# Optimization experiments

Hardware: AMD Instinct MI355X
Metric: run time of the kernel (lower is better)

## Reference

```python
import jax, jax.numpy as jnp
import numpy as np

N_NODES = 100000
N_EDGES = 3200000
N_FEAT = 512
HIDDEN = 16
OUT_DIM = 1


def setup_inputs() -> dict:
    key = jax.random.key(0)
    ks = jax.random.split(key, 6)
    x = jax.random.normal(ks[0], (N_NODES, N_FEAT), dtype=jnp.float32)
    lap_vals = jax.random.uniform(ks[1], (N_EDGES,), dtype=jnp.float32)
    W1 = jax.random.normal(ks[2], (N_FEAT, HIDDEN), dtype=jnp.float32) * 0.05
    b1 = jnp.zeros((HIDDEN,), dtype=jnp.float32)
    W2 = jax.random.normal(ks[3], (HIDDEN, OUT_DIM), dtype=jnp.float32) * 0.05
    b2 = jnp.zeros((OUT_DIM,), dtype=jnp.float32)
    lap_rows = jax.random.randint(ks[4], (N_EDGES,), 0, N_NODES, dtype=jnp.int32)
    lap_cols = jax.random.randint(ks[5], (N_EDGES,), 0, N_NODES, dtype=jnp.int32)
    return {"x": x, "lap_vals": lap_vals, "W1": W1, "b1": b1,
            "W2": W2, "b2": b2, "lap_rows": lap_rows, "lap_cols": lap_cols}


def _spmm(vals, rows, cols, dense):
    # COO sparse [N,N] @ dense [N,D]: gather source rows, scale, scatter-add.
    return jax.ops.segment_sum(vals[:, None] * dense[cols], rows,
                               num_segments=N_NODES)


def reference(x, lap_vals, W1, b1, W2, b2, lap_rows, lap_cols):
    # Layer 1: dense GEMM -> sparse aggregation -> fused bias + relu
    h = jax.nn.relu(_spmm(lap_vals, lap_rows, lap_cols, x @ W1) + b1)
    # Layer 2: dense GEMM -> sparse aggregation -> fused bias + sigmoid
    out = jax.nn.sigmoid(_spmm(lap_vals, lap_rows, lap_cols, h @ W2) + b2)
    return out
```

## Files before the change

kernel.cpp:

```cpp
#include <hip/hip_runtime.h>
#include <cstdint>
#include <cstddef>

#define N_NODES 100000
#define N_EDGES 3200000
#define N_FEAT  512
#define HIDDEN  16
#define NBUCK   ((N_NODES + 127) / 128)
#define BCAP    4608
#define CHUNK   2048
#define NGB     ((N_NODES + 63) / 64)
#define NBS     ((N_EDGES + CHUNK - 1) / CHUNK)
#define AGG_T   512

static_assert(NGB == NBS, "parity interleave requires equal role counts");

__device__ __forceinline__ void gload_lds16(const float* g, void* lds) {
  __builtin_amdgcn_global_load_lds(
      (const __attribute__((address_space(1))) void*)g,
      (__attribute__((address_space(3))) void*)lds, 16, 0, 0);
}

__global__ __launch_bounds__(256)
void k_prep(int* __restrict__ cursor) {
  const int i = blockIdx.x * 256 + threadIdx.x;
  if (i < NBUCK) cursor[i] = 0;
}

__global__ __launch_bounds__(256)
void k_mega2(const float* __restrict__ x, const float* __restrict__ W1,
             float* __restrict__ xw, const int* __restrict__ rows,
             const int* __restrict__ cols, const float* __restrict__ vals,
             int* __restrict__ cursor, int2* __restrict__ binned) {
  __shared__ __align__(16) char smem[32768];
  const int t = threadIdx.x;

  if ((blockIdx.x & 1) == 0) {
    float4 (*xs)[2][256] = reinterpret_cast<float4 (*)[2][256]>(smem);
    const int l = t & 63;
    const int w = __builtin_amdgcn_readfirstlane(t >> 6);
    const int rbase = (blockIdx.x >> 1) * 64;
    const int kbase0 = w * 128;

    float acc[16];
#pragma unroll
    for (int c = 0; c < 16; ++c) acc[c] = 0.f;

    const int sq   = ((l & 3) ^ ((l >> 3) & 3)) * 4;
    const int srow = l >> 2;

    auto STAGE = [&](int b, int ck) {
      const int kb = kbase0 + ck * 16;
#pragma unroll
      for (int i = 0; i < 4; ++i) {
        int grow = rbase + i * 16 + srow;
        if (grow >= N_NODES) grow = N_NODES - 1;
        gload_lds16(x + (size_t)grow * N_FEAT + kb + sq, &xs[w][b][i * 64]);
      }
    };

    const int rsw = (l >> 1) & 3;
    auto COMPUTE = [&](int b, int ck) {
      const int kb = kbase0 + ck * 16;
#pragma unroll
      for (int q = 0; q < 4; ++q) {
        float4 xv = xs[w][b][l * 4 + (q ^ rsw)];
        float xe[4] = {xv.x, xv.y, xv.z, xv.w};
#pragma unroll
        for (int j = 0; j < 4; ++j) {
          const float* wrow = W1 + (size_t)(kb + q * 4 + j) * 16;
#pragma unroll
          for (int c = 0; c < 16; ++c)
            acc[c] = fmaf(xe[j], wrow[c], acc[c]);
        }
      }
    };

    STAGE(0, 0);
#pragma unroll 1
    for (int ck = 0; ck < 8; ++ck) {
      const int b = ck & 1;
      if (ck + 1 < 8) {
        STAGE(b ^ 1, ck + 1);
        asm volatile("s_waitcnt vmcnt(4)" ::: "memory");
      } else {
        asm volatile("s_waitcnt vmcnt(0)" ::: "memory");
      }
      COMPUTE(b, ck);
    }

    float4* red = &xs[w][0][0];
    red[l * 4 + (0 ^ rsw)] = make_float4(acc[0],  acc[1],  acc[2],  acc[3]);
    red[l * 4 + (1 ^ rsw)] = make_float4(acc[4],  acc[5],  acc[6],  acc[7]);
    red[l * 4 + (2 ^ rsw)] = make_float4(acc[8],  acc[9],  acc[10], acc[11]);
    red[l * 4 + (3 ^ rsw)] = make_float4(acc[12], acc[13], acc[14], acc[15]);
    __syncthreads();

    const int rr = t >> 2, qq = t & 3;
    const int grow = rbase + rr;
    if (grow < N_NODES) {
      const int s = rr * 4 + (qq ^ ((rr >> 1) & 3));
      float4 a = xs[0][0][s], b4 = xs[1][0][s], c4 = xs[2][0][s], d4 = xs[3][0][s];
      float4 o = make_float4(a.x + b4.x + c4.x + d4.x, a.y + b4.y + c4.y + d4.y,
                             a.z + b4.z + c4.z + d4.z, a.w + b4.w + c4.w + d4.w);
      ((float4*)xw)[(size_t)grow * 4 + qq] = o;
    }
  } else {
    int2*           stash = (int2*)smem;
    unsigned short* sbuck = (unsigned short*)(smem + 16384);
    int*            hist  = (int*)(smem + 16384 + 4096);
    int*            base  = (int*)(smem + 16384 + 4096 + 4 * NBUCK);
    const int e0 = (blockIdx.x >> 1) * CHUNK;
    const int nv = (N_EDGES - e0 < CHUNK) ? (N_EDGES - e0) : CHUNK;

    for (int b = t; b < NBUCK; b += 256) hist[b] = 0;
    __syncthreads();

#pragma unroll
    for (int i = 0; i < CHUNK / 256; ++i) {
      const int idx = i * 256 + t;
      if (idx < nv) {
        const int e = e0 + idx;
        const int r = rows[e], c = cols[e];
        const float v = vals[e];
        const int b = r >> 7;
        stash[idx] = make_int2(c | ((r & 127) << 20), __float_as_int(v));
        sbuck[idx] = (unsigned short)b;
        atomicAdd(&hist[b], 1);
      }
    }
    __syncthreads();

    for (int b = t; b < NBUCK; b += 256) {
      const int h = hist[b];
      base[b] = (h > 0) ? atomicAdd(&cursor[b], h) : 0;
      hist[b] = 0;
    }
    __syncthreads();

#pragma unroll
    for (int i = 0; i < CHUNK / 256; ++i) {
      const int idx = i * 256 + t;
      if (idx < nv) {
        const int b = sbuck[idx];
        const int off = base[b] + atomicAdd(&hist[b], 1);
        if (off < BCAP) binned[(size_t)b * BCAP + off] = stash[idx];
      }
    }
  }
}

__global__ __launch_bounds__(AGG_T)
void k_sortagg(const int2* __restrict__ binned, const int* __restrict__ cursor,
               int2* __restrict__ binned2, int* __restrict__ row_beg,
               int* __restrict__ row_end, const float* __restrict__ xw,
               const float* __restrict__ b1, const float* __restrict__ W2,
               float* __restrict__ hw1) {
  __shared__ int2 stash[BCAP];
  __shared__ int hist[128];
  __shared__ int inc[128];
  __shared__ int cnt2[128];
  const int t = threadIdx.x;
  const int b = blockIdx.x;
  const int raw = cursor[b];
  const int cnt = raw < BCAP ? raw : BCAP;
  const int2* ep = binned + (size_t)b * BCAP;

  if (t < 128) { hist[t] = 0; cnt2[t] = 0; }
  __syncthreads();

  for (int i = t; i < cnt; i += AGG_T)
    atomicAdd(&hist[(ep[i].x >> 20) & 127], 1);
  __syncthreads();

  if (t < 128) inc[t] = hist[t];
  __syncthreads();
#pragma unroll
  for (int off = 1; off < 128; off <<= 1) {
    int add = (t >= off && t < 128) ? inc[t - off] : 0;
    __syncthreads();
    if (t < 128) inc[t] += add;
    __syncthreads();
  }

  if (t < 128) {
    const int r = b * 128 + t;
    if (r < N_NODES) {
      row_beg[r] = b * BCAP + inc[t] - hist[t];
      row_end[r] = b * BCAP + inc[t];
    }
  }

  for (int i = t; i < cnt; i += AGG_T) {
    const int2 e = ep[i];
    const int row = (e.x >> 20) & 127;
    const int off = inc[row] - hist[row] + atomicAdd(&cnt2[row], 1);
    stash[off] = e;
  }
  __syncthreads();

  int2* eq = binned2 + (size_t)b * BCAP;
  for (int i = t; i < cnt; i += AGG_T) eq[i] = stash[i];

  const int lane16 = t & 15;
  const int g = t >> 4;
  const float bb = b1[lane16];
  const float ww = W2[lane16];
#pragma unroll 1
  for (int rr = g; rr < 128; rr += 32) {
    const int r = b * 128 + rr;
    if (r >= N_NODES) continue;
    const int s = inc[rr] - hist[rr], e2 = inc[rr];
    float a0 = 0.f, a1 = 0.f, a2 = 0.f, a3 = 0.f;
    int i = s;
    for (; i + 3 < e2; i += 4) {
      int2 ea = stash[i],     eb = stash[i + 1];
      int2 ec = stash[i + 2], ed = stash[i + 3];
      a0 = fmaf(__int_as_float(ea.y), xw[(size_t)(ea.x & 0xFFFFF) * 16 + lane16], a0);
      a1 = fmaf(__int_as_float(eb.y), xw[(size_t)(eb.x & 0xFFFFF) * 16 + lane16], a1);
      a2 = fmaf(__int_as_float(ec.y), xw[(size_t)(ec.x & 0xFFFFF) * 16 + lane16], a2);
      a3 = fmaf(__int_as_float(ed.y), xw[(size_t)(ed.x & 0xFFFFF) * 16 + lane16], a3);
    }
    for (; i < e2; ++i) {
      int2 ea = stash[i];
      a0 = fmaf(__int_as_float(ea.y), xw[(size_t)(ea.x & 0xFFFFF) * 16 + lane16], a0);
    }
    float h = fmaxf((a0 + a1) + (a2 + a3) + bb, 0.f);
    float p = h * ww;
#pragma unroll
    for (int m = 8; m >= 1; m >>= 1) p += __shfl_xor(p, m, 16);
    if (lane16 == 0) hw1[r] = p;
  }
}

__global__ __launch_bounds__(256)
void k_fused2(const int2* __restrict__ binned2, const int* __restrict__ row_beg,
              const int* __restrict__ row_end, const float* __restrict__ hw1,
              const float* __restrict__ b2, float* __restrict__ out) {
  const int t = threadIdx.x;
  const int lane16 = t & 15;
  const int r = blockIdx.x * 16 + (t >> 4);
  if (r >= N_NODES) return;
  const int s = row_beg[r], e = row_end[r];
  float acc = 0.f;
  for (int i = s + lane16; i < e; i += 16) {
    int2 ev = binned2[i];
    acc = fmaf(__int_as_float(ev.y), hw1[ev.x & 0xFFFFF], acc);
  }
#pragma unroll
  for (int m = 8; m >= 1; m >>= 1) acc += __shfl_xor(acc, m, 16);
  if (lane16 == 0) out[r] = 1.f / (1.f + expf(-(acc + b2[0])));
}

extern "C" void kernel_launch(void* const* d_in, const int* in_sizes, int n_in,
                              void* d_out, int out_size, void* d_ws, size_t ws_size,
                              hipStream_t stream) {
  const float* x    = (const float*)d_in[0];
  const float* vals = (const float*)d_in[1];
  const float* W1   = (const float*)d_in[2];
  const float* b1   = (const float*)d_in[3];
  const float* W2   = (const float*)d_in[4];
  const float* b2   = (const float*)d_in[5];
  const int*   rows = (const int*)d_in[6];
  const int*   cols = (const int*)d_in[7];
  float* out = (float*)d_out;

  char* w = (char*)d_ws;
  float* xw      = (float*)w;  w += (size_t)N_NODES * 16 * 4;
  int2*  binned  = (int2*)w;   w += (size_t)NBUCK * BCAP * 8;
  int2*  binned2 = (int2*)w;   w += (size_t)NBUCK * BCAP * 8;
  int*   cursor  = (int*)w;    w += (size_t)((NBUCK + 3) & ~3) * 4;
  int*   row_beg = (int*)w;    w += (size_t)N_NODES * 4;
  int*   row_end = (int*)w;    w += (size_t)N_NODES * 4;
  float* hw1     = (float*)w;

  k_prep    <<<(NBUCK + 255) / 256, 256,   0, stream>>>(cursor);
  k_mega2   <<<NGB + NBS,           256,   0, stream>>>(x, W1, xw, rows, cols,
                                                        vals, cursor, binned);
  k_sortagg <<<NBUCK,               AGG_T, 0, stream>>>(binned, cursor, binned2,
                                                        row_beg, row_end, xw,
                                                        b1, W2, hw1);
  k_fused2  <<<(N_NODES + 15) / 16, 256,   0, stream>>>(binned2, row_beg, row_end,
                                                        hw1, b2, out);
}
```

Baseline: 156.2 us.

## Drop sorted edge copy; aggregate layer 2 via LDS atomics over buckets

```diff
diff --git a/kernel.cpp b/kernel.cpp
--- a/kernel.cpp
+++ b/kernel.cpp
@@ -152,10 +152,8 @@
 
 __global__ __launch_bounds__(AGG_T)
 void k_sortagg(const int2* __restrict__ binned, const int* __restrict__ cursor,
-               int2* __restrict__ binned2, int* __restrict__ row_beg,
-               int* __restrict__ row_end, const float* __restrict__ xw,
-               const float* __restrict__ b1, const float* __restrict__ W2,
-               float* __restrict__ hw1) {
+               const float* __restrict__ xw, const float* __restrict__ b1,
+               const float* __restrict__ W2, float* __restrict__ hw1) {
   __shared__ int2 stash[BCAP];
   __shared__ int hist[128];
   __shared__ int inc[128];
@@ -183,14 +181,6 @@
     __syncthreads();
   }
 
-  if (t < 128) {
-    const int r = b * 128 + t;
-    if (r < N_NODES) {
-      row_beg[r] = b * BCAP + inc[t] - hist[t];
-      row_end[r] = b * BCAP + inc[t];
-    }
-  }
-
   for (int i = t; i < cnt; i += AGG_T) {
     const int2 e = ep[i];
     const int row = (e.x >> 20) & 127;
@@ -198,9 +188,6 @@
     stash[off] = e;
   }
   __syncthreads();
-
-  int2* eq = binned2 + (size_t)b * BCAP;
-  for (int i = t; i < cnt; i += AGG_T) eq[i] = stash[i];
 
   const int lane16 = t & 15;
   const int g = t >> 4;
@@ -233,23 +220,39 @@
   }
 }
 
-__global__ __launch_bounds__(256)
-void k_fused2(const int2* __restrict__ binned2, const int* __restrict__ row_beg,
-              const int* __restrict__ row_end, const float* __restrict__ hw1,
-              const float* __restrict__ b2, float* __restrict__ out) {
+__global__ __launch_bounds__(AGG_T)
+void k_agg2(const int2* __restrict__ binned, const int* __restrict__ cursor,
+            const float* __restrict__ hw1, const float* __restrict__ b2,
+            float* __restrict__ out) {
+  __shared__ float acc2[128];
   const int t = threadIdx.x;
-  const int lane16 = t & 15;
-  const int r = blockIdx.x * 16 + (t >> 4);
-  if (r >= N_NODES) return;
-  const int s = row_beg[r], e = row_end[r];
-  float acc = 0.f;
-  for (int i = s + lane16; i < e; i += 16) {
-    int2 ev = binned2[i];
-    acc = fmaf(__int_as_float(ev.y), hw1[ev.x & 0xFFFFF], acc);
-  }
-#pragma unroll
-  for (int m = 8; m >= 1; m >>= 1) acc += __shfl_xor(acc, m, 16);
-  if (lane16 == 0) out[r] = 1.f / (1.f + expf(-(acc + b2[0])));
+  const int b = blockIdx.x;
+  if (t < 128) acc2[t] = 0.f;
+  __syncthreads();
+
+  const int raw = cursor[b];
+  const int cnt = raw < BCAP ? raw : BCAP;
+  const int2* ep = binned + (size_t)b * BCAP;
+
+  int i = t;
+  for (; i + AGG_T < cnt; i += 2 * AGG_T) {
+    const int2 ea = ep[i], eb = ep[i + AGG_T];
+    const float va = __int_as_float(ea.y) * hw1[ea.x & 0xFFFFF];
+    const float vb = __int_as_float(eb.y) * hw1[eb.x & 0xFFFFF];
+    atomicAdd(&acc2[(ea.x >> 20) & 127], va);
+    atomicAdd(&acc2[(eb.x >> 20) & 127], vb);
+  }
+  for (; i < cnt; i += AGG_T) {
+    const int2 ea = ep[i];
+    atomicAdd(&acc2[(ea.x >> 20) & 127],
+              __int_as_float(ea.y) * hw1[ea.x & 0xFFFFF]);
+  }
+  __syncthreads();
+
+  if (t < 128) {
+    const int r = b * 128 + t;
+    if (r < N_NODES) out[r] = 1.f / (1.f + expf(-(acc2[t] + b2[0])));
+  }
 }
 
 extern "C" void kernel_launch(void* const* d_in, const int* in_sizes, int n_in,
@@ -266,20 +269,16 @@
   float* out = (float*)d_out;
 
   char* w = (char*)d_ws;
-  float* xw      = (float*)w;  w += (size_t)N_NODES * 16 * 4;
-  int2*  binned  = (int2*)w;   w += (size_t)NBUCK * BCAP * 8;
-  int2*  binned2 = (int2*)w;   w += (size_t)NBUCK * BCAP * 8;
-  int*   cursor  = (int*)w;    w += (size_t)((NBUCK + 3) & ~3) * 4;
-  int*   row_beg = (int*)w;    w += (size_t)N_NODES * 4;
-  int*   row_end = (int*)w;    w += (size_t)N_NODES * 4;
-  float* hw1     = (float*)w;
+  float* xw     = (float*)w;  w += (size_t)N_NODES * 16 * 4;
+  int2*  binned = (int2*)w;   w += (size_t)NBUCK * BCAP * 8;
+  int*   cursor = (int*)w;    w += (size_t)((NBUCK + 3) & ~3) * 4;
+  float* hw1    = (float*)w;
 
   k_prep    <<<(NBUCK + 255) / 256, 256,   0, stream>>>(cursor);
   k_mega2   <<<NGB + NBS,           256,   0, stream>>>(x, W1, xw, rows, cols,
                                                         vals, cursor, binned);
-  k_sortagg <<<NBUCK,               AGG_T, 0, stream>>>(binned, cursor, binned2,
-                                                        row_beg, row_end, xw,
+  k_sortagg <<<NBUCK,               AGG_T, 0, stream>>>(binned, cursor, xw,
                                                         b1, W2, hw1);
-  k_fused2  <<<(N_NODES + 15) / 16, 256,   0, stream>>>(binned2, row_beg, row_end,
-                                                        hw1, b2, out);
-}
+  k_agg2    <<<NBUCK,               AGG_T, 0, stream>>>(binned, cursor, hw1,
+                                                        b2, out);
+}
```

New measurement: 157.6 us. No clear change (+0.9%).
